# Kernel optimization log

Hardware: AMD Instinct MI355X
Metric: run time of the kernel (lower is better)

Reference implementation:

```python
import jax, jax.numpy as jnp
import numpy as np

CHEB_K = 3

def avwgcn(x, E, w_pool, b_pool):
    # x: [B,N,C], E: [N,D], w_pool: [D,K,C,O], b_pool: [D,O]
    N = E.shape[0]
    supports = jax.nn.softmax(jax.nn.relu(E @ E.T), axis=1)  # [N,N]
    slist = [jnp.eye(N, dtype=x.dtype), supports]
    for _ in range(CHEB_K - 2):
        slist.append(2.0 * supports @ slist[-1] - slist[-2])
    S = jnp.stack(slist)                         # [K,N,N]
    W = jnp.einsum('nd,dkio->nkio', E, w_pool)   # [N,K,C,O]
    b = E @ b_pool                               # [N,O]
    xg = jnp.einsum('knm,bmc->bnkc', S, x)       # [B,N,K,C]
    return jnp.einsum('bnki,nkio->bno', xg, W) + b


def setup_inputs() -> dict:
    key = jax.random.key(0)
    ks = jax.random.split(key, 9)
    B, N, C_IN, C_OUT, D = 16, 2048, 64, 64, 10
    x = jax.random.normal(ks[0], (B, N, C_IN), dtype=jnp.float32)
    state = jax.random.normal(ks[1], (B, N, C_OUT), dtype=jnp.float32)
    node_embeddings = jax.random.normal(ks[2], (N, D), dtype=jnp.float32)
    gate_wpool = jax.random.normal(ks[3], (D, CHEB_K, C_IN + C_OUT, 2 * C_OUT), dtype=jnp.float32) * 0.1
    gate_bpool = jax.random.normal(ks[4], (D, 2 * C_OUT), dtype=jnp.float32) * 0.1
    upd_wpool = jax.random.normal(ks[5], (D, CHEB_K, C_IN + C_OUT, C_OUT), dtype=jnp.float32) * 0.1
    upd_bpool = jax.random.normal(ks[6], (D, C_OUT), dtype=jnp.float32) * 0.1
    lin_w = jax.random.normal(ks[7], (64, 128), dtype=jnp.float32) * 0.1
    lin_b = jax.random.normal(ks[8], (64,), dtype=jnp.float32) * 0.1
    return {"x": x, "state": state, "node_embeddings": node_embeddings,
            "gate_wpool": gate_wpool, "gate_bpool": gate_bpool,
            "upd_wpool": upd_wpool, "upd_bpool": upd_bpool,
            "lin_w": lin_w, "lin_b": lin_b}


def reference(x, state, node_embeddings, gate_wpool, gate_bpool, upd_wpool, upd_bpool, lin_w, lin_b):
    input_and_state = jnp.concatenate([x, state], axis=-1)          # [B,N,128]
    z_r = jax.nn.sigmoid(avwgcn(input_and_state, node_embeddings, gate_wpool, gate_bpool))  # [B,N,128]
    z_r = z_r @ lin_w.T + lin_b                                     # [B,N,64]
    candidate = jnp.concatenate([x, z_r], axis=-1)                  # [B,N,128]
    hc = jnp.tanh(avwgcn(candidate, node_embeddings, upd_wpool, upd_bpool))  # [B,N,64]
    return hc
```

## Files before the change

kernel.cpp:

```cpp
#include <hip/hip_runtime.h>

typedef unsigned short u16;
typedef short s16x8 __attribute__((ext_vector_type(8)));
typedef _Float16 h16x8 __attribute__((ext_vector_type(8)));
typedef float f32x4 __attribute__((ext_vector_type(4)));
typedef u16 u16x4 __attribute__((ext_vector_type(4)));

#define DEV static __device__ __forceinline__

DEV u16 f2h(float x){ union { _Float16 h; u16 u; } v; v.h = (_Float16)x; return v.u; }
DEV float h2f(u16 u){ union { u16 u; _Float16 h; } v; v.u = u; return (float)v.h; }
DEV void split_h(float x, u16& h, u16& l){
    h = f2h(x);
    l = f2h(x - h2f(h));
}
DEV h16x8 H8(s16x8 v){ union { s16x8 s; h16x8 h; } u; u.s = v; return u.h; }
DEV f32x4 mfma16(s16x8 a, s16x8 b, f32x4 c){
    return __builtin_amdgcn_mfma_f32_16x16x32_f16(H8(a), H8(b), c, 0, 0, 0);
}

DEV int swz(int r, int m){ return (m & ~0x38) | ((((m >> 3) ^ r) & 7) << 3); }

DEV void gll16(const u16* g, u16* l){
    __builtin_amdgcn_global_load_lds((const __attribute__((address_space(1))) void*)g,
                                     (__attribute__((address_space(3))) void*)l, 16, 0, 0);
}

__global__ __launch_bounds__(256) void k_supports(const float* __restrict__ E,
                                                  u16* __restrict__ Sh, u16* __restrict__ Sl)
{
    const int n = blockIdx.x, tid = threadIdx.x;
    const int w = tid >> 6, lane = tid & 63;
    __shared__ float red[8];

    float en[10];
    #pragma unroll
    for (int d = 0; d < 10; d++) en[d] = E[n*10 + d];

    float v[8];
    #pragma unroll
    for (int i = 0; i < 8; i++){
        int m = tid + i*256;
        const float* em = E + m*10;
        float s = 0.f;
        #pragma unroll
        for (int d = 0; d < 10; d++) s += en[d]*em[d];
        v[i] = fmaxf(s, 0.f);
    }
    float mx = v[0];
    #pragma unroll
    for (int i = 1; i < 8; i++) mx = fmaxf(mx, v[i]);
    #pragma unroll
    for (int off = 32; off > 0; off >>= 1) mx = fmaxf(mx, __shfl_xor(mx, off));
    if (lane == 0) red[w] = mx;
    __syncthreads();
    mx = fmaxf(fmaxf(red[0], red[1]), fmaxf(red[2], red[3]));
    __syncthreads();

    float sum = 0.f;
    #pragma unroll
    for (int i = 0; i < 8; i++){ v[i] = __expf(v[i] - mx); sum += v[i]; }
    #pragma unroll
    for (int off = 32; off > 0; off >>= 1) sum += __shfl_xor(sum, off);
    if (lane == 0) red[4 + w] = sum;
    __syncthreads();
    sum = red[4] + red[5] + red[6] + red[7];
    float inv = 1.f / sum;

    #pragma unroll
    for (int i = 0; i < 8; i++){
        float p = v[i] * inv;
        u16 h, l; split_h(p, h, l);
        int m = tid + i*256;
        int ms = swz(n, m);
        Sh[n*2048 + ms] = h;
        Sl[n*2048 + ms] = l;
    }
}

__global__ __launch_bounds__(256) void k_prep(const float* __restrict__ E,
    const float* __restrict__ gwp, const float* __restrict__ gbp,
    const float* __restrict__ uwp, const float* __restrict__ ubp,
    const float* __restrict__ x,   const float* __restrict__ state,
    const float* __restrict__ lw,
    u16* __restrict__ wg, u16* __restrict__ wu,
    float* __restrict__ bg, float* __restrict__ bu,
    u16* __restrict__ xt, u16* __restrict__ lwt)
{
    long idx = (long)blockIdx.x*256 + threadIdx.x;
    if (idx < 491520){
        int kk = (int)(idx & 31);
        int o  = (int)((idx >> 5) & 127);
        int r2 = (int)(idx >> 12);
        int d = r2 % 10, jc = r2 / 10;
        int j = jc*32 + kk;
        int k = j >> 7, i = j & 127;
        float v = gwp[(((d*3 + k)*128) + i)*128 + o];
        wg[idx] = f2h(v);
    } else if (idx < 737280){
        long t = idx - 491520;
        int kk = (int)(t & 31);
        int o  = (int)((t >> 5) & 63);
        int r2 = (int)(t >> 11);
        int d = r2 % 10, jc = r2 / 10;
        int j = jc*32 + kk;
        int k = j >> 7, i = j & 127;
        float v = uwp[(((d*3 + k)*128) + i)*64 + o];
        wu[t] = f2h(v);
    } else if (idx < 999424){
        long t = idx - 737280; int n = (int)(t >> 7), o = (int)(t & 127);
        float s = 0.f;
        #pragma unroll
        for (int d = 0; d < 10; d++) s += E[n*10+d]*gbp[d*128+o];
        bg[t] = s;
    } else if (idx < 1130496){
        long t = idx - 999424; int n = (int)(t >> 6), o = (int)(t & 63);
        float s = 0.f;
        #pragma unroll
        for (int d = 0; d < 10; d++) s += E[n*10+d]*ubp[d*64+o];
        bu[t] = s;
    } else if (idx < 5324800){
        long t = idx - 1130496;
        int colG = (int)(t >> 11), m = (int)(t & 2047);
        int b = colG >> 7, c = colG & 127;
        float v = (c < 64) ? x[((long)(b*2048)+m)*64 + c]
                           : state[((long)(b*2048)+m)*64 + c - 64];
        xt[(long)colG*2048 + swz(colG, m)] = f2h(v);
    } else if (idx < 5332992){
        long t = idx - 5324800;
        lwt[t] = f2h(lw[t]);
    }
}

template<int EPI>
__global__ __launch_bounds__(256) void k_gemm(
    const u16* __restrict__ Ah, const u16* __restrict__ Al,
    const u16* __restrict__ Bt,
    u16* __restrict__ Ot, float* __restrict__ Orow,
    const u16* __restrict__ Xt)
{
    __shared__ __attribute__((aligned(16))) u16 AsH[2][64*64];
    __shared__ __attribute__((aligned(16))) u16 AsL[2][64*64];
    __shared__ __attribute__((aligned(16))) u16 Bs[2][128*64];
    const int tid = threadIdx.x;
    const int xc = blockIdx.x & 7, ii = blockIdx.x >> 3;
    const int bm = ((xc & 3)*8 + (ii & 7)) << 6;
    const int bn = ((xc >> 2)*8 + (ii >> 3)) << 7;
    const int w = tid >> 6, lane = tid & 63;
    const int wm = (w & 1) << 5;
    const int wn = (w >> 1) << 6;
    const int lr = lane & 15, lk = lane >> 4;

    const int srow = tid >> 3, scol = (tid & 7) << 3;
    const long a0 = (long)(bm + srow)*2048 + scol;
    const long a1 = a0 + 32*2048;
    const long b0 = (long)(bn + srow)*2048 + scol;
    const long b1 = b0 + 32*2048;
    const long b2 = b0 + 64*2048;
    const long b3 = b0 + 96*2048;
    const int l0 = tid*8, l1 = tid*8 + 2048;

    const int c0 = (lk ^ (lr & 7)) << 3;
    const int c1 = c0 ^ 32;

#define STAGE(B, K) do { \
        gll16(Ah + a0 + (K), &AsH[B][l0]); \
        gll16(Ah + a1 + (K), &AsH[B][l1]); \
        gll16(Al + a0 + (K), &AsL[B][l0]); \
        gll16(Al + a1 + (K), &AsL[B][l1]); \
        gll16(Bt + b0 + (K), &Bs[B][l0]); \
        gll16(Bt + b1 + (K), &Bs[B][l1]); \
        gll16(Bt + b2 + (K), &Bs[B][l0 + 4096]); \
        gll16(Bt + b3 + (K), &Bs[B][l1 + 4096]); \
    } while(0)

    f32x4 acc[2][4];
    const f32x4 Z4 = {0.f, 0.f, 0.f, 0.f};
    #pragma unroll
    for (int i = 0; i < 2; i++)
        #pragma unroll
        for (int j = 0; j < 4; j++) acc[i][j] = Z4;

    STAGE(0, 0);
    __syncthreads();
    int cur = 0;
    for (int k0 = 0; k0 < 2048; k0 += 64){
        if (k0 + 64 < 2048) STAGE(cur ^ 1, k0 + 64);
        const u16* ah = AsH[cur];
        const u16* al = AsL[cur];
        const u16* bs = Bs[cur];
        #pragma unroll
        for (int s2 = 0; s2 < 2; s2++){
            const int cc = s2 ? c1 : c0;
            s16x8 bfv[4], af[2];
            #pragma unroll
            for (int ni = 0; ni < 4; ni++)
                bfv[ni] = *(const s16x8*)&bs[(wn + ni*16 + lr)*64 + cc];
            #pragma unroll
            for (int mi = 0; mi < 2; mi++)
                af[mi] = *(const s16x8*)&ah[(wm + mi*16 + lr)*64 + cc];
            #pragma unroll
            for (int mi = 0; mi < 2; mi++)
                #pragma unroll
                for (int ni = 0; ni < 4; ni++)
                    acc[mi][ni] = mfma16(af[mi], bfv[ni], acc[mi][ni]);
            #pragma unroll
            for (int mi = 0; mi < 2; mi++)
                af[mi] = *(const s16x8*)&al[(wm + mi*16 + lr)*64 + cc];
            #pragma unroll
            for (int mi = 0; mi < 2; mi++)
                #pragma unroll
                for (int ni = 0; ni < 4; ni++)
                    acc[mi][ni] = mfma16(af[mi], bfv[ni], acc[mi][ni]);
        }
        __syncthreads();
        cur ^= 1;
    }
#undef STAGE

    #pragma unroll
    for (int mi = 0; mi < 2; mi++){
        #pragma unroll
        for (int ni = 0; ni < 4; ni++){
            int i0 = bm + wm + mi*16 + lk*4;
            int j  = bn + wn + ni*16 + lr;
            f32x4 v = acc[mi][ni];
            if constexpr (EPI){
                u16x4 xh = *(const u16x4*)(Xt + (long)j*2048 + swz(j, i0));
                #pragma unroll
                for (int r = 0; r < 4; r++)
                    v[r] = 2.f*v[r] - h2f(xh[r]);
            }
            int bb = j >> 7, cc = j & 127;
            float* rp = Orow + ((long)bb*2048 + i0)*128 + cc;
            #pragma unroll
            for (int r = 0; r < 4; r++) rp[(long)r*128] = v[r];
            if constexpr (!EPI){
                u16x4 oh;
                #pragma unroll
                for (int r = 0; r < 4; r++) oh[r] = f2h(v[r]);
                *(u16x4*)(Ot + (long)j*2048 + swz(j, i0)) = oh;
            }
        }
    }
}

template<int OFULL, int ACT, int FUSE>
__global__ __launch_bounds__(256, 2) void k_combine(
    const float* __restrict__ G1r, const float* __restrict__ G2r,
    const float* __restrict__ x, const float* __restrict__ second,
    const u16* __restrict__ W,
    const float* __restrict__ bias, const float* __restrict__ E,
    float* __restrict__ out, u16* __restrict__ XtT,
    const u16* __restrict__ lwt, const float* __restrict__ lb)
{
    constexpr int NO = OFULL/32;
    __shared__ u16 Ash[64*40], Asl[64*40];
    __shared__ float Et[640];
    __shared__ u16 Zh[FUSE ? 64*136 : 1];
    __shared__ u16 Zl[FUSE ? 64*136 : 1];
    const int tid = threadIdx.x, bid = blockIdx.x;
    const int b = bid >> 5, n0 = (bid & 31) << 6;
    const int w = tid >> 6, lane = tid & 63;
    const int wm = (w & 1)*32, wo = (w >> 1)*(OFULL/2);
    const int lr = lane & 15, lk = lane >> 4;

    for (int i = tid; i < 640; i += 256)
        Et[i] = E[(n0 + (i & 63))*10 + (i >> 6)];

    const f32x4 Z4 = {0.f, 0.f, 0.f, 0.f};
    f32x4 acc[2][NO];
    #pragma unroll
    for (int mi = 0; mi < 2; mi++)
        #pragma unroll
        for (int oi = 0; oi < NO; oi++) acc[mi][oi] = Z4;

    const long rowbase = (long)b*2048 + n0;
    const int laneoff = (wo + lr)*32 + lk*8;

    s16x8 pbh[3][NO];

    for (int jc = 0; jc < 12; jc++){
        {
            const long t0 = (long)(jc*10 + 0)*OFULL*32;
            const long t1 = (long)(jc*10 + 1)*OFULL*32;
            #pragma unroll
            for (int oi = 0; oi < NO; oi++){
                pbh[0][oi] = *(const s16x8*)(W + t0 + laneoff + oi*16*32);
                pbh[1][oi] = *(const s16x8*)(W + t1 + laneoff + oi*16*32);
            }
        }
        __syncthreads();
        {
            const float* src; int stride;
            if (jc < 4){
                int col0 = jc*32;
                src = (col0 < 64) ? (x + rowbase*64 + col0)
                                  : (second + rowbase*64 + (col0 - 64));
                stride = 64;
            } else if (jc < 8){
                src = G1r + rowbase*128 + (jc-4)*32; stride = 128;
            } else {
                src = G2r + rowbase*128 + (jc-8)*32; stride = 128;
            }
            int row = tid >> 2, c8 = (tid & 3)*8;
            f32x4 s0 = *(const f32x4*)(src + (long)row*stride + c8);
            f32x4 s1 = *(const f32x4*)(src + (long)row*stride + c8 + 4);
            s16x8 vh, vl;
            #pragma unroll
            for (int t = 0; t < 4; t++){
                u16 h,l; split_h(s0[t], h, l); vh[t]=(short)h; vl[t]=(short)l;
            }
            #pragma unroll
            for (int t = 0; t < 4; t++){
                u16 h,l; split_h(s1[t], h, l); vh[4+t]=(short)h; vl[4+t]=(short)l;
            }
            *(s16x8*)&Ash[row*40 + c8] = vh;
            *(s16x8*)&Asl[row*40 + c8] = vl;
        }
        __syncthreads();

        s16x8 ah[2], al[2];
        #pragma unroll
        for (int mi = 0; mi < 2; mi++){
            ah[mi] = *(const s16x8*)&Ash[(wm + mi*16 + lr)*40 + lk*8];
            al[mi] = *(const s16x8*)&Asl[(wm + mi*16 + lr)*40 + lk*8];
        }

        #pragma unroll
        for (int d = 0; d < 10; d++){
            const int cur = d % 3;
            if (d < 8){
                const int nx = (d + 2) % 3;
                const long t2 = (long)(jc*10 + d + 2)*OFULL*32;
                #pragma unroll
                for (int oi = 0; oi < NO; oi++)
                    pbh[nx][oi] = *(const s16x8*)(W + t2 + laneoff + oi*16*32);
            }
            f32x4 Cd[2][NO];
            #pragma unroll
            for (int mi = 0; mi < 2; mi++)
                #pragma unroll
                for (int oi = 0; oi < NO; oi++)
                    Cd[mi][oi] = mfma16(ah[mi], pbh[cur][oi], Z4);
            #pragma unroll
            for (int mi = 0; mi < 2; mi++)
                #pragma unroll
                for (int oi = 0; oi < NO; oi++)
                    Cd[mi][oi] = mfma16(al[mi], pbh[cur][oi], Cd[mi][oi]);
            #pragma unroll
            for (int mi = 0; mi < 2; mi++){
                f32x4 e4 = *(const f32x4*)&Et[d*64 + wm + mi*16 + lk*4];
                #pragma unroll
                for (int oi = 0; oi < NO; oi++) acc[mi][oi] += e4 * Cd[mi][oi];
            }
        }
    }

    if constexpr (!FUSE){
        #pragma unroll
        for (int mi = 0; mi < 2; mi++){
            #pragma unroll
            for (int oi = 0; oi < NO; oi++){
                int mrow = n0 + wm + mi*16 + lk*4;
                int o = wo + oi*16 + lr;
                #pragma unroll
                for (int r = 0; r < 4; r++){
                    float v = acc[mi][oi][r] + bias[(long)(mrow + r)*OFULL + o];
                    v = (ACT == 0) ? (1.f/(1.f + __expf(-v))) : tanhf(v);
                    out[((long)b*2048 + mrow + r)*OFULL + o] = v;
                }
            }
        }
    } else {
        #pragma unroll
        for (int mi = 0; mi < 2; mi++){
            #pragma unroll
            for (int oi = 0; oi < NO; oi++){
                int lrow = wm + mi*16 + lk*4;
                int o = wo + oi*16 + lr;
                #pragma unroll
                for (int r = 0; r < 4; r++){
                    float v = acc[mi][oi][r] + bias[(long)(n0 + lrow + r)*OFULL + o];
                    v = 1.f/(1.f + __expf(-v));
                    u16 h, l; split_h(v, h, l);
                    Zh[(lrow + r)*136 + o] = h;
                    Zl[(lrow + r)*136 + o] = l;
                }
            }
        }
        __syncthreads();
        f32x4 az[4];
        #pragma unroll
        for (int mi = 0; mi < 4; mi++) az[mi] = Z4;
        const int oz = w*16 + lr;
        #pragma unroll
        for (int ks = 0; ks < 4; ks++){
            s16x8 bw = *(const s16x8*)(lwt + oz*128 + ks*32 + lk*8);
            #pragma unroll
            for (int mi = 0; mi < 4; mi++){
                s16x8 zh = *(const s16x8*)&Zh[(mi*16 + lr)*136 + ks*32 + lk*8];
                az[mi] = mfma16(zh, bw, az[mi]);
            }
            #pragma unroll
            for (int mi = 0; mi < 4; mi++){
                s16x8 zl = *(const s16x8*)&Zl[(mi*16 + lr)*136 + ks*32 + lk*8];
                az[mi] = mfma16(zl, bw, az[mi]);
            }
        }
        const float lbv = lb[w*16 + lr];
        const int colG = b*128 + 64 + w*16 + lr;
        #pragma unroll
        for (int mi = 0; mi < 4; mi++){
            int mrow = n0 + mi*16 + lk*4;
            u16x4 tq;
            #pragma unroll
            for (int r = 0; r < 4; r++){
                float v = az[mi][r] + lbv;
                out[((long)b*2048 + mrow + r)*64 + w*16 + lr] = v;
                tq[r] = f2h(v);
            }
            *(u16x4*)(XtT + (long)colG*2048 + swz(colG, mrow)) = tq;
        }
    }
}

extern "C" void kernel_launch(void* const* d_in, const int* in_sizes, int n_in,
                              void* d_out, int out_size, void* d_ws, size_t ws_size,
                              hipStream_t stream)
{
    const float* x   = (const float*)d_in[0];
    const float* st  = (const float*)d_in[1];
    const float* E   = (const float*)d_in[2];
    const float* gwp = (const float*)d_in[3];
    const float* gbp = (const float*)d_in[4];
    const float* uwp = (const float*)d_in[5];
    const float* ubp = (const float*)d_in[6];
    const float* lw  = (const float*)d_in[7];
    const float* lb  = (const float*)d_in[8];
    float* out = (float*)d_out;
    char* ws = (char*)d_ws;

    const size_t MB8 = 8388608;
    u16*   Sh   = (u16*)(ws);
    u16*   Sl   = (u16*)(ws + 1*MB8);
    u16*   Xt   = (u16*)(ws + 2*MB8);
    u16*   G1t  = (u16*)(ws + 3*MB8);
    float* G1row= (float*)(ws + 4*MB8);
    float* G2row= (float*)(ws + 6*MB8);
    float* zr   = (float*)(ws + 8*MB8);
    char*  p    = ws + 9*MB8;
    u16* wg = (u16*)p;             p += 983040;
    u16* wu = (u16*)p;             p += 491520;
    float* bg = (float*)p;         p += 1048576;
    float* bu = (float*)p;         p += 524288;
    u16* lwt = (u16*)p;            p += 16384;

    k_supports<<<dim3(2048), dim3(256), 0, stream>>>(E, Sh, Sl);
    k_prep<<<dim3(20832), dim3(256), 0, stream>>>(E, gwp, gbp, uwp, ubp, x, st, lw,
                                                  wg, wu, bg, bu, Xt, lwt);
    k_gemm<0><<<dim3(512), dim3(256), 0, stream>>>(Sh, Sl, Xt, G1t, G1row,
                                                   (const u16*)nullptr);
    k_gemm<1><<<dim3(512), dim3(256), 0, stream>>>(Sh, Sl, G1t, (u16*)nullptr, G2row,
                                                   Xt);
    k_combine<128,0,1><<<dim3(512), dim3(256), 0, stream>>>(G1row, G2row, x, st,
                                                            wg, bg, E, zr, Xt, lwt, lb);
    k_gemm<0><<<dim3(512), dim3(256), 0, stream>>>(Sh, Sl, Xt, G1t, G1row,
                                                   (const u16*)nullptr);
    k_gemm<1><<<dim3(512), dim3(256), 0, stream>>>(Sh, Sl, G1t, (u16*)nullptr, G2row,
                                                   Xt);
    k_combine<64,1,0><<<dim3(512), dim3(256), 0, stream>>>(G1row, G2row, x, zr,
                                                           wu, bu, E, out,
                                                           (u16*)nullptr,
                                                           (const u16*)nullptr,
                                                           (const float*)nullptr);
}
```

Measured before the change: 357.3 us.

## Store GEMM outputs as split fp16 pairs and double-buffer combine staging

```diff
diff --git a/kernel.cpp b/kernel.cpp
--- a/kernel.cpp
+++ b/kernel.cpp
@@ -20,62 +20,11 @@
 }
 
 DEV int swz(int r, int m){ return (m & ~0x38) | ((((m >> 3) ^ r) & 7) << 3); }
+DEV int swzG(int row, int c){ return (c & ~0x18) | ((((c >> 3) ^ (row >> 1)) & 3) << 3); }
 
 DEV void gll16(const u16* g, u16* l){
     __builtin_amdgcn_global_load_lds((const __attribute__((address_space(1))) void*)g,
                                      (__attribute__((address_space(3))) void*)l, 16, 0, 0);
-}
-
-__global__ __launch_bounds__(256) void k_supports(const float* __restrict__ E,
-                                                  u16* __restrict__ Sh, u16* __restrict__ Sl)
-{
-    const int n = blockIdx.x, tid = threadIdx.x;
-    const int w = tid >> 6, lane = tid & 63;
-    __shared__ float red[8];
-
-    float en[10];
-    #pragma unroll
-    for (int d = 0; d < 10; d++) en[d] = E[n*10 + d];
-
-    float v[8];
-    #pragma unroll
-    for (int i = 0; i < 8; i++){
-        int m = tid + i*256;
-        const float* em = E + m*10;
-        float s = 0.f;
-        #pragma unroll
-        for (int d = 0; d < 10; d++) s += en[d]*em[d];
-        v[i] = fmaxf(s, 0.f);
-    }
-    float mx = v[0];
-    #pragma unroll
-    for (int i = 1; i < 8; i++) mx = fmaxf(mx, v[i]);
-    #pragma unroll
-    for (int off = 32; off > 0; off >>= 1) mx = fmaxf(mx, __shfl_xor(mx, off));
-    if (lane == 0) red[w] = mx;
-    __syncthreads();
-    mx = fmaxf(fmaxf(red[0], red[1]), fmaxf(red[2], red[3]));
-    __syncthreads();
-
-    float sum = 0.f;
-    #pragma unroll
-    for (int i = 0; i < 8; i++){ v[i] = __expf(v[i] - mx); sum += v[i]; }
-    #pragma unroll
-    for (int off = 32; off > 0; off >>= 1) sum += __shfl_xor(sum, off);
-    if (lane == 0) red[4 + w] = sum;
-    __syncthreads();
-    sum = red[4] + red[5] + red[6] + red[7];
-    float inv = 1.f / sum;
-
-    #pragma unroll
-    for (int i = 0; i < 8; i++){
-        float p = v[i] * inv;
-        u16 h, l; split_h(p, h, l);
-        int m = tid + i*256;
-        int ms = swz(n, m);
-        Sh[n*2048 + ms] = h;
-        Sl[n*2048 + ms] = l;
-    }
 }
 
 __global__ __launch_bounds__(256) void k_prep(const float* __restrict__ E,
@@ -85,9 +34,56 @@
     const float* __restrict__ lw,
     u16* __restrict__ wg, u16* __restrict__ wu,
     float* __restrict__ bg, float* __restrict__ bu,
-    u16* __restrict__ xt, u16* __restrict__ lwt)
+    u16* __restrict__ xt, u16* __restrict__ lwt,
+    u16* __restrict__ Sh, u16* __restrict__ Sl)
 {
-    long idx = (long)blockIdx.x*256 + threadIdx.x;
+    __shared__ float red[8];
+    const int tid = threadIdx.x;
+    if (blockIdx.x < 2048){
+        const int n = blockIdx.x;
+        const int w = tid >> 6, lane = tid & 63;
+        float en[10];
+        #pragma unroll
+        for (int d = 0; d < 10; d++) en[d] = E[n*10 + d];
+        float v[8];
+        #pragma unroll
+        for (int i = 0; i < 8; i++){
+            int m = tid + i*256;
+            const float* em = E + m*10;
+            float s = 0.f;
+            #pragma unroll
+            for (int d = 0; d < 10; d++) s += en[d]*em[d];
+            v[i] = fmaxf(s, 0.f);
+        }
+        float mx = v[0];
+        #pragma unroll
+        for (int i = 1; i < 8; i++) mx = fmaxf(mx, v[i]);
+        #pragma unroll
+        for (int off = 32; off > 0; off >>= 1) mx = fmaxf(mx, __shfl_xor(mx, off));
+        if (lane == 0) red[w] = mx;
+        __syncthreads();
+        mx = fmaxf(fmaxf(red[0], red[1]), fmaxf(red[2], red[3]));
+        __syncthreads();
+        float sum = 0.f;
+        #pragma unroll
+        for (int i = 0; i < 8; i++){ v[i] = __expf(v[i] - mx); sum += v[i]; }
+        #pragma unroll
+        for (int off = 32; off > 0; off >>= 1) sum += __shfl_xor(sum, off);
+        if (lane == 0) red[4 + w] = sum;
+        __syncthreads();
+        sum = red[4] + red[5] + red[6] + red[7];
+        float inv = 1.f / sum;
+        #pragma unroll
+        for (int i = 0; i < 8; i++){
+            float p = v[i] * inv;
+            u16 h, l; split_h(p, h, l);
+            int ms = swz(n, tid + i*256);
+            Sh[n*2048 + ms] = h;
+            Sl[n*2048 + ms] = l;
+        }
+        return;
+    }
+    long idx = (long)(blockIdx.x - 2048)*256 + tid;
     if (idx < 491520){
         int kk = (int)(idx & 31);
         int o  = (int)((idx >> 5) & 127);
@@ -136,7 +132,7 @@
 __global__ __launch_bounds__(256) void k_gemm(
     const u16* __restrict__ Ah, const u16* __restrict__ Al,
     const u16* __restrict__ Bt,
-    u16* __restrict__ Ot, float* __restrict__ Orow,
+    u16* __restrict__ Ot, u16* __restrict__ Gh, u16* __restrict__ Gl,
     const u16* __restrict__ Xt)
 {
     __shared__ __attribute__((aligned(16))) u16 AsH[2][64*64];
@@ -232,9 +228,14 @@
                     v[r] = 2.f*v[r] - h2f(xh[r]);
             }
             int bb = j >> 7, cc = j & 127;
-            float* rp = Orow + ((long)bb*2048 + i0)*128 + cc;
-            #pragma unroll
-            for (int r = 0; r < 4; r++) rp[(long)r*128] = v[r];
+            long gbase = ((long)bb*2048 + i0)*128;
+            #pragma unroll
+            for (int r = 0; r < 4; r++){
+                int cs = swzG(i0 + r, cc);
+                u16 gh, gl; split_h(v[r], gh, gl);
+                Gh[gbase + (long)r*128 + cs] = gh;
+                Gl[gbase + (long)r*128 + cs] = gl;
+            }
             if constexpr (!EPI){
                 u16x4 oh;
                 #pragma unroll
@@ -247,7 +248,8 @@
 
 template<int OFULL, int ACT, int FUSE>
 __global__ __launch_bounds__(256, 2) void k_combine(
-    const float* __restrict__ G1r, const float* __restrict__ G2r,
+    const u16* __restrict__ G1h, const u16* __restrict__ G1l,
+    const u16* __restrict__ G2h, const u16* __restrict__ G2l,
     const float* __restrict__ x, const float* __restrict__ second,
     const u16* __restrict__ W,
     const float* __restrict__ bias, const float* __restrict__ E,
@@ -255,7 +257,8 @@
     const u16* __restrict__ lwt, const float* __restrict__ lb)
 {
     constexpr int NO = OFULL/32;
-    __shared__ u16 Ash[64*40], Asl[64*40];
+    __shared__ __attribute__((aligned(16))) u16 Ash[2][64*32];
+    __shared__ __attribute__((aligned(16))) u16 Asl[2][64*32];
     __shared__ float Et[640];
     __shared__ u16 Zh[FUSE ? 64*136 : 1];
     __shared__ u16 Zl[FUSE ? 64*136 : 1];
@@ -278,9 +281,44 @@
     const long rowbase = (long)b*2048 + n0;
     const int laneoff = (wo + lr)*32 + lk*8;
 
+    const int srow = tid >> 2, schunk = tid & 3;
+    const int sg = (srow >> 1) & 3;
+    const int sdstV = srow*32 + ((schunk ^ sg) << 3);
+    const int ldst  = tid*8;
+
+    const int fco = (lk ^ ((lr >> 1) & 3)) << 3;
+
+    auto stageV = [&](int jc, int buf){
+        int col0 = jc*32;
+        const float* src = (col0 < 64) ? (x + rowbase*64 + col0)
+                                       : (second + rowbase*64 + (col0 - 64));
+        src += (long)srow*64 + schunk*8;
+        f32x4 s0 = *(const f32x4*)src;
+        f32x4 s1 = *(const f32x4*)(src + 4);
+        s16x8 vh, vl;
+        #pragma unroll
+        for (int t = 0; t < 4; t++){ u16 h,l; split_h(s0[t],h,l); vh[t]=(short)h; vl[t]=(short)l; }
+        #pragma unroll
+        for (int t = 0; t < 4; t++){ u16 h,l; split_h(s1[t],h,l); vh[4+t]=(short)h; vl[4+t]=(short)l; }
+        *(s16x8*)&Ash[buf][sdstV] = vh;
+        *(s16x8*)&Asl[buf][sdstV] = vl;
+    };
+    auto stageG = [&](int jc, int buf){
+        const u16 *sh, *sl; int col0;
+        if (jc < 8){ sh = G1h; sl = G1l; col0 = (jc-4)*32; }
+        else       { sh = G2h; sl = G2l; col0 = (jc-8)*32; }
+        long off = (rowbase + srow)*128 + col0 + schunk*8;
+        gll16(sh + off, &Ash[buf][ldst]);
+        gll16(sl + off, &Asl[buf][ldst]);
+    };
+
+    stageV(0, 0);
+    __syncthreads();
+
     s16x8 pbh[3][NO];
 
     for (int jc = 0; jc < 12; jc++){
+        const int cb = jc & 1;
         {
             const long t0 = (long)(jc*10 + 0)*OFULL*32;
             const long t1 = (long)(jc*10 + 1)*OFULL*32;
@@ -290,41 +328,15 @@
                 pbh[1][oi] = *(const s16x8*)(W + t1 + laneoff + oi*16*32);
             }
         }
-        __syncthreads();
-        {
-            const float* src; int stride;
-            if (jc < 4){
-                int col0 = jc*32;
-                src = (col0 < 64) ? (x + rowbase*64 + col0)
-                                  : (second + rowbase*64 + (col0 - 64));
-                stride = 64;
-            } else if (jc < 8){
-                src = G1r + rowbase*128 + (jc-4)*32; stride = 128;
-            } else {
-                src = G2r + rowbase*128 + (jc-8)*32; stride = 128;
-            }
-            int row = tid >> 2, c8 = (tid & 3)*8;
-            f32x4 s0 = *(const f32x4*)(src + (long)row*stride + c8);
-            f32x4 s1 = *(const f32x4*)(src + (long)row*stride + c8 + 4);
-            s16x8 vh, vl;
-            #pragma unroll
-            for (int t = 0; t < 4; t++){
-                u16 h,l; split_h(s0[t], h, l); vh[t]=(short)h; vl[t]=(short)l;
-            }
-            #pragma unroll
-            for (int t = 0; t < 4; t++){
-                u16 h,l; split_h(s1[t], h, l); vh[4+t]=(short)h; vl[4+t]=(short)l;
-            }
-            *(s16x8*)&Ash[row*40 + c8] = vh;
-            *(s16x8*)&Asl[row*40 + c8] = vl;
-        }
-        __syncthreads();
-
+        if (jc < 11){
+            if (jc + 1 < 4) stageV(jc + 1, cb ^ 1);
+            else            stageG(jc + 1, cb ^ 1);
+        }
         s16x8 ah[2], al[2];
         #pragma unroll
         for (int mi = 0; mi < 2; mi++){
-            ah[mi] = *(const s16x8*)&Ash[(wm + mi*16 + lr)*40 + lk*8];
-            al[mi] = *(const s16x8*)&Asl[(wm + mi*16 + lr)*40 + lk*8];
+            ah[mi] = *(const s16x8*)&Ash[cb][(wm + mi*16 + lr)*32 + fco];
+            al[mi] = *(const s16x8*)&Asl[cb][(wm + mi*16 + lr)*32 + fco];
         }
 
         #pragma unroll
@@ -355,6 +367,7 @@
                 for (int oi = 0; oi < NO; oi++) acc[mi][oi] += e4 * Cd[mi][oi];
             }
         }
+        __syncthreads();
     }
 
     if constexpr (!FUSE){
@@ -446,8 +459,10 @@
     u16*   Sl   = (u16*)(ws + 1*MB8);
     u16*   Xt   = (u16*)(ws + 2*MB8);
     u16*   G1t  = (u16*)(ws + 3*MB8);
-    float* G1row= (float*)(ws + 4*MB8);
-    float* G2row= (float*)(ws + 6*MB8);
+    u16*   G1h  = (u16*)(ws + 4*MB8);
+    u16*   G1l  = (u16*)(ws + 5*MB8);
+    u16*   G2h  = (u16*)(ws + 6*MB8);
+    u16*   G2l  = (u16*)(ws + 7*MB8);
     float* zr   = (float*)(ws + 8*MB8);
     char*  p    = ws + 9*MB8;
     u16* wg = (u16*)p;             p += 983040;
@@ -456,21 +471,21 @@
     float* bu = (float*)p;         p += 524288;
     u16* lwt = (u16*)p;            p += 16384;
 
-    k_supports<<<dim3(2048), dim3(256), 0, stream>>>(E, Sh, Sl);
-    k_prep<<<dim3(20832), dim3(256), 0, stream>>>(E, gwp, gbp, uwp, ubp, x, st, lw,
-                                                  wg, wu, bg, bu, Xt, lwt);
-    k_gemm<0><<<dim3(512), dim3(256), 0, stream>>>(Sh, Sl, Xt, G1t, G1row,
+    k_prep<<<dim3(22880), dim3(256), 0, stream>>>(E, gwp, gbp, uwp, ubp, x, st, lw,
+                                                  wg, wu, bg, bu, Xt, lwt, Sh, Sl);
+    k_gemm<0><<<dim3(512), dim3(256), 0, stream>>>(Sh, Sl, Xt, G1t, G1h, G1l,
                                                    (const u16*)nullptr);
-    k_gemm<1><<<dim3(512), dim3(256), 0, stream>>>(Sh, Sl, G1t, (u16*)nullptr, G2row,
-                                                   Xt);
-    k_combine<128,0,1><<<dim3(512), dim3(256), 0, stream>>>(G1row, G2row, x, st,
-                                                            wg, bg, E, zr, Xt, lwt, lb);
-    k_gemm<0><<<dim3(512), dim3(256), 0, stream>>>(Sh, Sl, Xt, G1t, G1row,
+    k_gemm<1><<<dim3(512), dim3(256), 0, stream>>>(Sh, Sl, G1t, (u16*)nullptr,
+                                                   G2h, G2l, Xt);
+    k_combine<128,0,1><<<dim3(512), dim3(256), 0, stream>>>(G1h, G1l, G2h, G2l,
+                                                            x, st, wg, bg, E,
+                                                            zr, Xt, lwt, lb);
+    k_gemm<0><<<dim3(512), dim3(256), 0, stream>>>(Sh, Sl, Xt, G1t, G1h, G1l,
                                                    (const u16*)nullptr);
-    k_gemm<1><<<dim3(512), dim3(256), 0, stream>>>(Sh, Sl, G1t, (u16*)nullptr, G2row,
-                                                   Xt);
-    k_combine<64,1,0><<<dim3(512), dim3(256), 0, stream>>>(G1row, G2row, x, zr,
-                                                           wu, bu, E, out,
+    k_gemm<1><<<dim3(512), dim3(256), 0, stream>>>(Sh, Sl, G1t, (u16*)nullptr,
+                                                   G2h, G2l, Xt);
+    k_combine<64,1,0><<<dim3(512), dim3(256), 0, stream>>>(G1h, G1l, G2h, G2l,
+                                                           x, zr, wu, bu, E, out,
                                                            (u16*)nullptr,
                                                            (const u16*)nullptr,
                                                            (const float*)nullptr);
```

New measurement: 365.5 us. 2.3% more time.

## Load GEMM A operand directly to registers and fuse supports into prep kernel

Applied to the files above, without the earlier changes.

```diff
diff --git a/kernel.cpp b/kernel.cpp
--- a/kernel.cpp
+++ b/kernel.cpp
@@ -24,58 +24,6 @@
 DEV void gll16(const u16* g, u16* l){
     __builtin_amdgcn_global_load_lds((const __attribute__((address_space(1))) void*)g,
                                      (__attribute__((address_space(3))) void*)l, 16, 0, 0);
-}
-
-__global__ __launch_bounds__(256) void k_supports(const float* __restrict__ E,
-                                                  u16* __restrict__ Sh, u16* __restrict__ Sl)
-{
-    const int n = blockIdx.x, tid = threadIdx.x;
-    const int w = tid >> 6, lane = tid & 63;
-    __shared__ float red[8];
-
-    float en[10];
-    #pragma unroll
-    for (int d = 0; d < 10; d++) en[d] = E[n*10 + d];
-
-    float v[8];
-    #pragma unroll
-    for (int i = 0; i < 8; i++){
-        int m = tid + i*256;
-        const float* em = E + m*10;
-        float s = 0.f;
-        #pragma unroll
-        for (int d = 0; d < 10; d++) s += en[d]*em[d];
-        v[i] = fmaxf(s, 0.f);
-    }
-    float mx = v[0];
-    #pragma unroll
-    for (int i = 1; i < 8; i++) mx = fmaxf(mx, v[i]);
-    #pragma unroll
-    for (int off = 32; off > 0; off >>= 1) mx = fmaxf(mx, __shfl_xor(mx, off));
-    if (lane == 0) red[w] = mx;
-    __syncthreads();
-    mx = fmaxf(fmaxf(red[0], red[1]), fmaxf(red[2], red[3]));
-    __syncthreads();
-
-    float sum = 0.f;
-    #pragma unroll
-    for (int i = 0; i < 8; i++){ v[i] = __expf(v[i] - mx); sum += v[i]; }
-    #pragma unroll
-    for (int off = 32; off > 0; off >>= 1) sum += __shfl_xor(sum, off);
-    if (lane == 0) red[4 + w] = sum;
-    __syncthreads();
-    sum = red[4] + red[5] + red[6] + red[7];
-    float inv = 1.f / sum;
-
-    #pragma unroll
-    for (int i = 0; i < 8; i++){
-        float p = v[i] * inv;
-        u16 h, l; split_h(p, h, l);
-        int m = tid + i*256;
-        int ms = swz(n, m);
-        Sh[n*2048 + ms] = h;
-        Sl[n*2048 + ms] = l;
-    }
 }
 
 __global__ __launch_bounds__(256) void k_prep(const float* __restrict__ E,
@@ -85,9 +33,56 @@
     const float* __restrict__ lw,
     u16* __restrict__ wg, u16* __restrict__ wu,
     float* __restrict__ bg, float* __restrict__ bu,
-    u16* __restrict__ xt, u16* __restrict__ lwt)
+    u16* __restrict__ xt, u16* __restrict__ lwt,
+    u16* __restrict__ Sh, u16* __restrict__ Sl)
 {
-    long idx = (long)blockIdx.x*256 + threadIdx.x;
+    __shared__ float red[8];
+    const int tid = threadIdx.x;
+    if (blockIdx.x < 2048){
+        const int n = blockIdx.x;
+        const int w = tid >> 6, lane = tid & 63;
+        float en[10];
+        #pragma unroll
+        for (int d = 0; d < 10; d++) en[d] = E[n*10 + d];
+        float v[8];
+        #pragma unroll
+        for (int i = 0; i < 8; i++){
+            int m = tid + i*256;
+            const float* em = E + m*10;
+            float s = 0.f;
+            #pragma unroll
+            for (int d = 0; d < 10; d++) s += en[d]*em[d];
+            v[i] = fmaxf(s, 0.f);
+        }
+        float mx = v[0];
+        #pragma unroll
+        for (int i = 1; i < 8; i++) mx = fmaxf(mx, v[i]);
+        #pragma unroll
+        for (int off = 32; off > 0; off >>= 1) mx = fmaxf(mx, __shfl_xor(mx, off));
+        if (lane == 0) red[w] = mx;
+        __syncthreads();
+        mx = fmaxf(fmaxf(red[0], red[1]), fmaxf(red[2], red[3]));
+        __syncthreads();
+        float sum = 0.f;
+        #pragma unroll
+        for (int i = 0; i < 8; i++){ v[i] = __expf(v[i] - mx); sum += v[i]; }
+        #pragma unroll
+        for (int off = 32; off > 0; off >>= 1) sum += __shfl_xor(sum, off);
+        if (lane == 0) red[4 + w] = sum;
+        __syncthreads();
+        sum = red[4] + red[5] + red[6] + red[7];
+        float inv = 1.f / sum;
+        #pragma unroll
+        for (int i = 0; i < 8; i++){
+            float p = v[i] * inv;
+            u16 h, l; split_h(p, h, l);
+            int ms = swz(n, tid + i*256);
+            Sh[n*2048 + ms] = h;
+            Sl[n*2048 + ms] = l;
+        }
+        return;
+    }
+    long idx = (long)(blockIdx.x - 2048)*256 + tid;
     if (idx < 491520){
         int kk = (int)(idx & 31);
         int o  = (int)((idx >> 5) & 127);
@@ -139,8 +134,6 @@
     u16* __restrict__ Ot, float* __restrict__ Orow,
     const u16* __restrict__ Xt)
 {
-    __shared__ __attribute__((aligned(16))) u16 AsH[2][64*64];
-    __shared__ __attribute__((aligned(16))) u16 AsL[2][64*64];
     __shared__ __attribute__((aligned(16))) u16 Bs[2][128*64];
     const int tid = threadIdx.x;
     const int xc = blockIdx.x & 7, ii = blockIdx.x >> 3;
@@ -152,8 +145,6 @@
     const int lr = lane & 15, lk = lane >> 4;
 
     const int srow = tid >> 3, scol = (tid & 7) << 3;
-    const long a0 = (long)(bm + srow)*2048 + scol;
-    const long a1 = a0 + 32*2048;
     const long b0 = (long)(bn + srow)*2048 + scol;
     const long b1 = b0 + 32*2048;
     const long b2 = b0 + 64*2048;
@@ -163,15 +154,54 @@
     const int c0 = (lk ^ (lr & 7)) << 3;
     const int c1 = c0 ^ 32;
 
-#define STAGE(B, K) do { \
-        gll16(Ah + a0 + (K), &AsH[B][l0]); \
-        gll16(Ah + a1 + (K), &AsH[B][l1]); \
-        gll16(Al + a0 + (K), &AsL[B][l0]); \
-        gll16(Al + a1 + (K), &AsL[B][l1]); \
-        gll16(Bt + b0 + (K), &Bs[B][l0]); \
-        gll16(Bt + b1 + (K), &Bs[B][l1]); \
-        gll16(Bt + b2 + (K), &Bs[B][l0 + 4096]); \
-        gll16(Bt + b3 + (K), &Bs[B][l1 + 4096]); \
+    const long ab0 = (long)(bm + wm + lr)*2048;
+    const long ab1 = ab0 + 16*2048;
+
+#define STAGEB(BUF, K) do { \
+        gll16(Bt + b0 + (K), &Bs[BUF][l0]); \
+        gll16(Bt + b1 + (K), &Bs[BUF][l1]); \
+        gll16(Bt + b2 + (K), &Bs[BUF][l0 + 4096]); \
+        gll16(Bt + b3 + (K), &Bs[BUF][l1 + 4096]); \
+    } while(0)
+
+#define LOADA(P, K) do { \
+        P##h00 = *(const s16x8*)(Ah + ab0 + (K) + c0); \
+        P##h01 = *(const s16x8*)(Ah + ab0 + (K) + c1); \
+        P##h10 = *(const s16x8*)(Ah + ab1 + (K) + c0); \
+        P##h11 = *(const s16x8*)(Ah + ab1 + (K) + c1); \
+        P##l00 = *(const s16x8*)(Al + ab0 + (K) + c0); \
+        P##l01 = *(const s16x8*)(Al + ab0 + (K) + c1); \
+        P##l10 = *(const s16x8*)(Al + ab1 + (K) + c0); \
+        P##l11 = *(const s16x8*)(Al + ab1 + (K) + c1); \
+    } while(0)
+
+#define HALF(BUF, CC, AH0, AH1, AL0, AL1) do { \
+        const u16* bs_ = Bs[BUF]; \
+        s16x8 bv0 = *(const s16x8*)&bs_[(wn +  0 + lr)*64 + (CC)]; \
+        s16x8 bv1 = *(const s16x8*)&bs_[(wn + 16 + lr)*64 + (CC)]; \
+        s16x8 bv2 = *(const s16x8*)&bs_[(wn + 32 + lr)*64 + (CC)]; \
+        s16x8 bv3 = *(const s16x8*)&bs_[(wn + 48 + lr)*64 + (CC)]; \
+        acc[0][0] = mfma16(AH0, bv0, acc[0][0]); \
+        acc[0][1] = mfma16(AH0, bv1, acc[0][1]); \
+        acc[0][2] = mfma16(AH0, bv2, acc[0][2]); \
+        acc[0][3] = mfma16(AH0, bv3, acc[0][3]); \
+        acc[1][0] = mfma16(AH1, bv0, acc[1][0]); \
+        acc[1][1] = mfma16(AH1, bv1, acc[1][1]); \
+        acc[1][2] = mfma16(AH1, bv2, acc[1][2]); \
+        acc[1][3] = mfma16(AH1, bv3, acc[1][3]); \
+        acc[0][0] = mfma16(AL0, bv0, acc[0][0]); \
+        acc[0][1] = mfma16(AL0, bv1, acc[0][1]); \
+        acc[0][2] = mfma16(AL0, bv2, acc[0][2]); \
+        acc[0][3] = mfma16(AL0, bv3, acc[0][3]); \
+        acc[1][0] = mfma16(AL1, bv0, acc[1][0]); \
+        acc[1][1] = mfma16(AL1, bv1, acc[1][1]); \
+        acc[1][2] = mfma16(AL1, bv2, acc[1][2]); \
+        acc[1][3] = mfma16(AL1, bv3, acc[1][3]); \
+    } while(0)
+
+#define STEP(P, BUF) do { \
+        HALF(BUF, c0, P##h00, P##h10, P##l00, P##l10); \
+        HALF(BUF, c1, P##h01, P##h11, P##l01, P##l11); \
     } while(0)
 
     f32x4 acc[2][4];
@@ -181,42 +211,25 @@
         #pragma unroll
         for (int j = 0; j < 4; j++) acc[i][j] = Z4;
 
-    STAGE(0, 0);
+    s16x8 Xh00,Xh01,Xh10,Xh11,Xl00,Xl01,Xl10,Xl11;
+    s16x8 Yh00,Yh01,Yh10,Yh11,Yl00,Yl01,Yl10,Yl11;
+
+    STAGEB(0, 0);
+    LOADA(X, 0);
     __syncthreads();
-    int cur = 0;
-    for (int k0 = 0; k0 < 2048; k0 += 64){
-        if (k0 + 64 < 2048) STAGE(cur ^ 1, k0 + 64);
-        const u16* ah = AsH[cur];
-        const u16* al = AsL[cur];
-        const u16* bs = Bs[cur];
-        #pragma unroll
-        for (int s2 = 0; s2 < 2; s2++){
-            const int cc = s2 ? c1 : c0;
-            s16x8 bfv[4], af[2];
-            #pragma unroll
-            for (int ni = 0; ni < 4; ni++)
-                bfv[ni] = *(const s16x8*)&bs[(wn + ni*16 + lr)*64 + cc];
-            #pragma unroll
-            for (int mi = 0; mi < 2; mi++)
-                af[mi] = *(const s16x8*)&ah[(wm + mi*16 + lr)*64 + cc];
-            #pragma unroll
-            for (int mi = 0; mi < 2; mi++)
-                #pragma unroll
-                for (int ni = 0; ni < 4; ni++)
-                    acc[mi][ni] = mfma16(af[mi], bfv[ni], acc[mi][ni]);
-            #pragma unroll
-            for (int mi = 0; mi < 2; mi++)
-                af[mi] = *(const s16x8*)&al[(wm + mi*16 + lr)*64 + cc];
-            #pragma unroll
-            for (int mi = 0; mi < 2; mi++)
-                #pragma unroll
-                for (int ni = 0; ni < 4; ni++)
-                    acc[mi][ni] = mfma16(af[mi], bfv[ni], acc[mi][ni]);
-        }
-        __syncthreads();
-        cur ^= 1;
-    }
-#undef STAGE
+    #pragma unroll 1
+    for (int k0 = 0; k0 < 2048; k0 += 128){
+        if (k0 + 64 < 2048){ STAGEB(1, k0 + 64); LOADA(Y, k0 + 64); }
+        STEP(X, 0);
+        __syncthreads();
+        if (k0 + 128 < 2048){ STAGEB(0, k0 + 128); LOADA(X, k0 + 128); }
+        STEP(Y, 1);
+        __syncthreads();
+    }
+#undef STAGEB
+#undef LOADA
+#undef HALF
+#undef STEP
 
     #pragma unroll
     for (int mi = 0; mi < 2; mi++){
@@ -456,9 +469,8 @@
     float* bu = (float*)p;         p += 524288;
     u16* lwt = (u16*)p;            p += 16384;
 
-    k_supports<<<dim3(2048), dim3(256), 0, stream>>>(E, Sh, Sl);
-    k_prep<<<dim3(20832), dim3(256), 0, stream>>>(E, gwp, gbp, uwp, ubp, x, st, lw,
-                                                  wg, wu, bg, bu, Xt, lwt);
+    k_prep<<<dim3(22880), dim3(256), 0, stream>>>(E, gwp, gbp, uwp, ubp, x, st, lw,
+                                                  wg, wu, bg, bu, Xt, lwt, Sh, Sl);
     k_gemm<0><<<dim3(512), dim3(256), 0, stream>>>(Sh, Sl, Xt, G1t, G1row,
                                                    (const u16*)nullptr);
     k_gemm<1><<<dim3(512), dim3(256), 0, stream>>>(Sh, Sl, G1t, (u16*)nullptr, G2row,
```

New measurement: 411.9 us. +15.3%, slower.

## Fold supports softmax into prep kernel and split each GEMM into two K-phase launches

Applied to the files above, without the earlier changes.

```diff
diff --git a/kernel.cpp b/kernel.cpp
--- a/kernel.cpp
+++ b/kernel.cpp
@@ -24,58 +24,6 @@
 DEV void gll16(const u16* g, u16* l){
     __builtin_amdgcn_global_load_lds((const __attribute__((address_space(1))) void*)g,
                                      (__attribute__((address_space(3))) void*)l, 16, 0, 0);
-}
-
-__global__ __launch_bounds__(256) void k_supports(const float* __restrict__ E,
-                                                  u16* __restrict__ Sh, u16* __restrict__ Sl)
-{
-    const int n = blockIdx.x, tid = threadIdx.x;
-    const int w = tid >> 6, lane = tid & 63;
-    __shared__ float red[8];
-
-    float en[10];
-    #pragma unroll
-    for (int d = 0; d < 10; d++) en[d] = E[n*10 + d];
-
-    float v[8];
-    #pragma unroll
-    for (int i = 0; i < 8; i++){
-        int m = tid + i*256;
-        const float* em = E + m*10;
-        float s = 0.f;
-        #pragma unroll
-        for (int d = 0; d < 10; d++) s += en[d]*em[d];
-        v[i] = fmaxf(s, 0.f);
-    }
-    float mx = v[0];
-    #pragma unroll
-    for (int i = 1; i < 8; i++) mx = fmaxf(mx, v[i]);
-    #pragma unroll
-    for (int off = 32; off > 0; off >>= 1) mx = fmaxf(mx, __shfl_xor(mx, off));
-    if (lane == 0) red[w] = mx;
-    __syncthreads();
-    mx = fmaxf(fmaxf(red[0], red[1]), fmaxf(red[2], red[3]));
-    __syncthreads();
-
-    float sum = 0.f;
-    #pragma unroll
-    for (int i = 0; i < 8; i++){ v[i] = __expf(v[i] - mx); sum += v[i]; }
-    #pragma unroll
-    for (int off = 32; off > 0; off >>= 1) sum += __shfl_xor(sum, off);
-    if (lane == 0) red[4 + w] = sum;
-    __syncthreads();
-    sum = red[4] + red[5] + red[6] + red[7];
-    float inv = 1.f / sum;
-
-    #pragma unroll
-    for (int i = 0; i < 8; i++){
-        float p = v[i] * inv;
-        u16 h, l; split_h(p, h, l);
-        int m = tid + i*256;
-        int ms = swz(n, m);
-        Sh[n*2048 + ms] = h;
-        Sl[n*2048 + ms] = l;
-    }
 }
 
 __global__ __launch_bounds__(256) void k_prep(const float* __restrict__ E,
@@ -85,9 +33,56 @@
     const float* __restrict__ lw,
     u16* __restrict__ wg, u16* __restrict__ wu,
     float* __restrict__ bg, float* __restrict__ bu,
-    u16* __restrict__ xt, u16* __restrict__ lwt)
+    u16* __restrict__ xt, u16* __restrict__ lwt,
+    u16* __restrict__ Sh, u16* __restrict__ Sl)
 {
-    long idx = (long)blockIdx.x*256 + threadIdx.x;
+    __shared__ float red[8];
+    const int tid = threadIdx.x;
+    if (blockIdx.x < 2048){
+        const int n = blockIdx.x;
+        const int w = tid >> 6, lane = tid & 63;
+        float en[10];
+        #pragma unroll
+        for (int d = 0; d < 10; d++) en[d] = E[n*10 + d];
+        float v[8];
+        #pragma unroll
+        for (int i = 0; i < 8; i++){
+            int m = tid + i*256;
+            const float* em = E + m*10;
+            float s = 0.f;
+            #pragma unroll
+            for (int d = 0; d < 10; d++) s += en[d]*em[d];
+            v[i] = fmaxf(s, 0.f);
+        }
+        float mx = v[0];
+        #pragma unroll
+        for (int i = 1; i < 8; i++) mx = fmaxf(mx, v[i]);
+        #pragma unroll
+        for (int off = 32; off > 0; off >>= 1) mx = fmaxf(mx, __shfl_xor(mx, off));
+        if (lane == 0) red[w] = mx;
+        __syncthreads();
+        mx = fmaxf(fmaxf(red[0], red[1]), fmaxf(red[2], red[3]));
+        __syncthreads();
+        float sum = 0.f;
+        #pragma unroll
+        for (int i = 0; i < 8; i++){ v[i] = __expf(v[i] - mx); sum += v[i]; }
+        #pragma unroll
+        for (int off = 32; off > 0; off >>= 1) sum += __shfl_xor(sum, off);
+        if (lane == 0) red[4 + w] = sum;
+        __syncthreads();
+        sum = red[4] + red[5] + red[6] + red[7];
+        float inv = 1.f / sum;
+        #pragma unroll
+        for (int i = 0; i < 8; i++){
+            float p = v[i] * inv;
+            u16 h, l; split_h(p, h, l);
+            int ms = swz(n, tid + i*256);
+            Sh[n*2048 + ms] = h;
+            Sl[n*2048 + ms] = l;
+        }
+        return;
+    }
+    long idx = (long)(blockIdx.x - 2048)*256 + tid;
     if (idx < 491520){
         int kk = (int)(idx & 31);
         int o  = (int)((idx >> 5) & 127);
@@ -132,7 +127,7 @@
     }
 }
 
-template<int EPI>
+template<int EPI, int PH>
 __global__ __launch_bounds__(256) void k_gemm(
     const u16* __restrict__ Ah, const u16* __restrict__ Al,
     const u16* __restrict__ Bt,
@@ -163,6 +158,8 @@
     const int c0 = (lk ^ (lr & 7)) << 3;
     const int c1 = c0 ^ 32;
 
+    constexpr int K0 = PH*1024, KEND = K0 + 1024;
+
 #define STAGE(B, K) do { \
         gll16(Ah + a0 + (K), &AsH[B][l0]); \
         gll16(Ah + a1 + (K), &AsH[B][l1]); \
@@ -175,17 +172,31 @@
     } while(0)
 
     f32x4 acc[2][4];
-    const f32x4 Z4 = {0.f, 0.f, 0.f, 0.f};
-    #pragma unroll
-    for (int i = 0; i < 2; i++)
-        #pragma unroll
-        for (int j = 0; j < 4; j++) acc[i][j] = Z4;
-
-    STAGE(0, 0);
+    if constexpr (PH == 0){
+        const f32x4 Z4 = {0.f, 0.f, 0.f, 0.f};
+        #pragma unroll
+        for (int i = 0; i < 2; i++)
+            #pragma unroll
+            for (int j = 0; j < 4; j++) acc[i][j] = Z4;
+    } else {
+        #pragma unroll
+        for (int mi = 0; mi < 2; mi++)
+            #pragma unroll
+            for (int ni = 0; ni < 4; ni++){
+                int i0 = bm + wm + mi*16 + lk*4;
+                int j  = bn + wn + ni*16 + lr;
+                int bb = j >> 7, cc = j & 127;
+                const float* rp = Orow + ((long)bb*2048 + i0)*128 + cc;
+                #pragma unroll
+                for (int r = 0; r < 4; r++) acc[mi][ni][r] = rp[(long)r*128];
+            }
+    }
+
+    STAGE(0, K0);
     __syncthreads();
     int cur = 0;
-    for (int k0 = 0; k0 < 2048; k0 += 64){
-        if (k0 + 64 < 2048) STAGE(cur ^ 1, k0 + 64);
+    for (int k0 = K0; k0 < KEND; k0 += 64){
+        if (k0 + 64 < KEND) STAGE(cur ^ 1, k0 + 64);
         const u16* ah = AsH[cur];
         const u16* al = AsL[cur];
         const u16* bs = Bs[cur];
@@ -225,7 +236,7 @@
             int i0 = bm + wm + mi*16 + lk*4;
             int j  = bn + wn + ni*16 + lr;
             f32x4 v = acc[mi][ni];
-            if constexpr (EPI){
+            if constexpr (PH == 1 && EPI){
                 u16x4 xh = *(const u16x4*)(Xt + (long)j*2048 + swz(j, i0));
                 #pragma unroll
                 for (int r = 0; r < 4; r++)
@@ -235,7 +246,7 @@
             float* rp = Orow + ((long)bb*2048 + i0)*128 + cc;
             #pragma unroll
             for (int r = 0; r < 4; r++) rp[(long)r*128] = v[r];
-            if constexpr (!EPI){
+            if constexpr (PH == 1 && !EPI){
                 u16x4 oh;
                 #pragma unroll
                 for (int r = 0; r < 4; r++) oh[r] = f2h(v[r]);
@@ -456,19 +467,26 @@
     float* bu = (float*)p;         p += 524288;
     u16* lwt = (u16*)p;            p += 16384;
 
-    k_supports<<<dim3(2048), dim3(256), 0, stream>>>(E, Sh, Sl);
-    k_prep<<<dim3(20832), dim3(256), 0, stream>>>(E, gwp, gbp, uwp, ubp, x, st, lw,
-                                                  wg, wu, bg, bu, Xt, lwt);
-    k_gemm<0><<<dim3(512), dim3(256), 0, stream>>>(Sh, Sl, Xt, G1t, G1row,
-                                                   (const u16*)nullptr);
-    k_gemm<1><<<dim3(512), dim3(256), 0, stream>>>(Sh, Sl, G1t, (u16*)nullptr, G2row,
-                                                   Xt);
+    k_prep<<<dim3(22880), dim3(256), 0, stream>>>(E, gwp, gbp, uwp, ubp, x, st, lw,
+                                                  wg, wu, bg, bu, Xt, lwt, Sh, Sl);
+    k_gemm<0,0><<<dim3(512), dim3(256), 0, stream>>>(Sh, Sl, Xt, G1t, G1row,
+                                                     (const u16*)nullptr);
+    k_gemm<0,1><<<dim3(512), dim3(256), 0, stream>>>(Sh, Sl, Xt, G1t, G1row,
+                                                     (const u16*)nullptr);
+    k_gemm<1,0><<<dim3(512), dim3(256), 0, stream>>>(Sh, Sl, G1t, (u16*)nullptr,
+                                                     G2row, Xt);
+    k_gemm<1,1><<<dim3(512), dim3(256), 0, stream>>>(Sh, Sl, G1t, (u16*)nullptr,
+                                                     G2row, Xt);
     k_combine<128,0,1><<<dim3(512), dim3(256), 0, stream>>>(G1row, G2row, x, st,
                                                             wg, bg, E, zr, Xt, lwt, lb);
-    k_gemm<0><<<dim3(512), dim3(256), 0, stream>>>(Sh, Sl, Xt, G1t, G1row,
-                                                   (const u16*)nullptr);
-    k_gemm<1><<<dim3(512), dim3(256), 0, stream>>>(Sh, Sl, G1t, (u16*)nullptr, G2row,
-                                                   Xt);
+    k_gemm<0,0><<<dim3(512), dim3(256), 0, stream>>>(Sh, Sl, Xt, G1t, G1row,
+                                                     (const u16*)nullptr);
+    k_gemm<0,1><<<dim3(512), dim3(256), 0, stream>>>(Sh, Sl, Xt, G1t, G1row,
+                                                     (const u16*)nullptr);
+    k_gemm<1,0><<<dim3(512), dim3(256), 0, stream>>>(Sh, Sl, G1t, (u16*)nullptr,
+                                                     G2row, Xt);
+    k_gemm<1,1><<<dim3(512), dim3(256), 0, stream>>>(Sh, Sl, G1t, (u16*)nullptr,
+                                                     G2row, Xt);
     k_combine<64,1,0><<<dim3(512), dim3(256), 0, stream>>>(G1row, G2row, x, zr,
                                                            wu, bu, E, out,
                                                            (u16*)nullptr,
```

Result: slower. 391.6 us (+9.6%).
